# Optimization experiments

Measured on AMD Instinct MI355X. Metric: run time of the kernel, lower is better.

Reference implementation:

```python
import jax, jax.numpy as jnp
import numpy as np

SEQ_LEN = 4_194_304  # number of tokens
INPUT_BITS = 16      # bits per token, MSB first


def setup_inputs() -> dict:
    key = jax.random.key(0)
    # bits in {0,1}; float32 carrier (values exact, matches uint8 bit semantics)
    tokens = jax.random.randint(key, (SEQ_LEN, INPUT_BITS), 0, 2).astype(jnp.float32)
    return {"tokens": tokens}


def reference(tokens):
    # tokens: [seq_len, input_bits], MSB first, entries in {0,1}
    bits = tokens.shape[1]
    # _bits_to_int: val = val*2 + b  ==  dot with [2^(bits-1), ..., 2, 1]
    pow2 = jnp.exp2(jnp.arange(bits - 1, -1, -1, dtype=jnp.float32))  # [bits]
    values = tokens @ pow2  # [seq_len], exact for bits <= 24
    # stable ascending sort == Python list.sort on (value, original_index)
    order = jnp.argsort(values, stable=True)  # [seq_len]
    return tokens[order]  # gather rows by rank
```

## Files before the change

### kernel.cpp

```cpp
#include <hip/hip_runtime.h>
#include <stdint.h>

static constexpr uint32_t SEQN = 4194304u;
static constexpr uint32_t BINS = 65536u;
static constexpr uint32_t QWORDS = BINS / 4u;
static constexpr uint32_t NBLK = 512u;
static constexpr uint32_t NTHR = 1024u;
static constexpr uint32_t ROWS_PER_BLK = SEQN / NBLK;
static constexpr uint32_t NSEG = 8u;

__global__ __launch_bounds__(NTHR) void k_hist_lds(const float4* __restrict__ in4,
                                                   uint32_t* __restrict__ partial) {
  __shared__ uint32_t h[QWORDS];
  uint32_t tid = threadIdx.x, blk = blockIdx.x;
  uint4* hv = (uint4*)h;
  for (uint32_t i = tid; i < QWORDS / 4u; i += NTHR) hv[i] = make_uint4(0u, 0u, 0u, 0u);
  __syncthreads();
  uint32_t row0 = blk * ROWS_PER_BLK;
#pragma unroll 2
  for (uint32_t r = row0 + tid; r < row0 + ROWS_PER_BLK; r += NTHR) {
    const float4* p = in4 + (size_t)r * 4u;
    float4 a = p[0], b = p[1], c = p[2], d = p[3];
    float kf = a.x;
    kf = kf * 2.0f + a.y; kf = kf * 2.0f + a.z; kf = kf * 2.0f + a.w;
    kf = kf * 2.0f + b.x; kf = kf * 2.0f + b.y; kf = kf * 2.0f + b.z; kf = kf * 2.0f + b.w;
    kf = kf * 2.0f + c.x; kf = kf * 2.0f + c.y; kf = kf * 2.0f + c.z; kf = kf * 2.0f + c.w;
    kf = kf * 2.0f + d.x; kf = kf * 2.0f + d.y; kf = kf * 2.0f + d.z; kf = kf * 2.0f + d.w;
    uint32_t key = (uint32_t)kf;
    atomicAdd(&h[key >> 2], 1u << ((key & 3u) << 3));
  }
  __syncthreads();
  uint4* dst = (uint4*)(partial + (size_t)blk * QWORDS);
  for (uint32_t i = tid; i < QWORDS / 4u; i += NTHR) dst[i] = hv[i];
}

__global__ __launch_bounds__(256) void k_reduceA(const uint32_t* __restrict__ partial,
                                                 uint2* __restrict__ seg) {
  uint32_t tid = threadIdx.x, blk = blockIdx.x;
  uint32_t s = blk >> 6, wg = blk & 63u;
  uint32_t w = wg * 256u + tid;
  uint32_t acc_e = 0u, acc_o = 0u;
  uint32_t p0 = s * (NBLK / NSEG);
#pragma unroll 8
  for (uint32_t p = p0; p < p0 + NBLK / NSEG; ++p) {
    uint32_t v = partial[(size_t)p * QWORDS + w];
    acc_e += v & 0x00FF00FFu;
    acc_o += (v >> 8) & 0x00FF00FFu;
  }
  seg[(size_t)s * QWORDS + w] = make_uint2(acc_e, acc_o);
}

__global__ __launch_bounds__(256) void k_scanA(const uint2* __restrict__ seg,
                                               uint32_t* __restrict__ hist,
                                               uint32_t* __restrict__ blkTot) {
  uint32_t tid = threadIdx.x, blk = blockIdx.x;
  uint32_t w = blk * 256u + tid;
  uint32_t e = 0u, o = 0u;
#pragma unroll
  for (uint32_t s = 0; s < NSEG; ++s) {
    uint2 v = seg[(size_t)s * QWORDS + w];
    e += v.x;
    o += v.y;
  }
  uint32_t c0 = e & 0xFFFFu, c2 = e >> 16, c1 = o & 0xFFFFu, c3 = o >> 16;
  ((uint4*)hist)[w] = make_uint4(c0, c1, c2, c3);
  uint32_t ssum = c0 + c1 + c2 + c3;
  for (int d = 1; d < 64; d <<= 1) ssum += __shfl_xor(ssum, d, 64);
  __shared__ uint32_t wt[4];
  if ((tid & 63u) == 0u) wt[tid >> 6] = ssum;
  __syncthreads();
  if (tid == 0u) blkTot[blk] = wt[0] + wt[1] + wt[2] + wt[3];
}

__global__ __launch_bounds__(256) void k_zero(uint32_t* __restrict__ hist) {
  uint32_t i = blockIdx.x * 256u + threadIdx.x;
  if (i < BINS) hist[i] = 0u;
}

__global__ __launch_bounds__(256) void k_hist(const float4* __restrict__ in4,
                                              uint32_t* __restrict__ hist) {
  uint32_t r = blockIdx.x * 256u + threadIdx.x;
  if (r >= SEQN) return;
  uint32_t key = 0u;
#pragma unroll
  for (uint32_t q = 0; q < 4u; ++q) {
    float4 v = in4[(size_t)r * 4u + q];
    uint32_t nib = ((uint32_t)v.x << 3) | ((uint32_t)v.y << 2) |
                   ((uint32_t)v.z << 1) | (uint32_t)v.w;
    key = (key << 4) | nib;
  }
  atomicAdd(&hist[key], 1u);
}

__global__ __launch_bounds__(256) void k_scan1(const uint32_t* __restrict__ hist,
                                               uint32_t* __restrict__ blkTot) {
  uint32_t tid = threadIdx.x, blk = blockIdx.x;
  uint32_t b0 = blk * 1024u + tid * 4u;
  uint32_t s = hist[b0] + hist[b0 + 1] + hist[b0 + 2] + hist[b0 + 3];
  for (int d = 1; d < 64; d <<= 1) s += __shfl_xor(s, d, 64);
  __shared__ uint32_t wt[4];
  if ((tid & 63u) == 0u) wt[tid >> 6] = s;
  __syncthreads();
  if (tid == 0u) blkTot[blk] = wt[0] + wt[1] + wt[2] + wt[3];
}

__global__ __launch_bounds__(64) void k_scan2(uint32_t* __restrict__ blkTot) {
  uint32_t t = threadIdx.x;
  uint32_t v = blkTot[t];
  uint32_t incl = v;
  for (int d = 1; d < 64; d <<= 1) {
    uint32_t n = __shfl_up(incl, d, 64);
    if (t >= (uint32_t)d) incl += n;
  }
  blkTot[t] = incl - v;
}

__global__ __launch_bounds__(256) void k_scan3(const uint32_t* __restrict__ hist,
                                               const uint32_t* __restrict__ blkBase,
                                               uint32_t* __restrict__ offs) {
  uint32_t tid = threadIdx.x, blk = blockIdx.x;
  uint32_t lane = tid & 63u, wid = tid >> 6;
  uint32_t b0 = blk * 1024u + tid * 4u;
  uint4 c = ((const uint4*)hist)[b0 >> 2];
  uint32_t s = c.x + c.y + c.z + c.w;
  uint32_t incl = s;
  for (int d = 1; d < 64; d <<= 1) {
    uint32_t n = __shfl_up(incl, d, 64);
    if (lane >= (uint32_t)d) incl += n;
  }
  __shared__ uint32_t wt[4];
  if (lane == 63u) wt[wid] = incl;
  __syncthreads();
  uint32_t wbase = 0u;
  for (uint32_t w = 0; w < wid; ++w) wbase += wt[w];
  uint32_t base = blkBase[blk] + wbase + (incl - s);
  ((uint4*)offs)[b0 >> 2] = make_uint4(base, base + c.x, base + c.x + c.y,
                                       base + c.x + c.y + c.z);
}

__global__ __launch_bounds__(256) void k_write(const uint32_t* __restrict__ hist,
                                               const uint32_t* __restrict__ offs,
                                               float4* __restrict__ out4) {
  __shared__ uint32_t s_off[32], s_cnt[32];
  uint32_t tid = threadIdx.x, blk = blockIdx.x;
  if (tid < 32u) {
    uint32_t k = blk * 32u + tid;
    s_off[tid] = offs[k];
    s_cnt[tid] = hist[k];
  }
  __syncthreads();
  uint32_t q = tid & 3u;
  for (uint32_t kk = 0; kk < 32u; ++kk) {
    uint32_t k = blk * 32u + kk;
    uint32_t off = s_off[kk], cnt = s_cnt[kk];
    float4 pat;
    pat.x = (float)((k >> (15u - (q * 4u + 0u))) & 1u);
    pat.y = (float)((k >> (15u - (q * 4u + 1u))) & 1u);
    pat.z = (float)((k >> (15u - (q * 4u + 2u))) & 1u);
    pat.w = (float)((k >> (15u - (q * 4u + 3u))) & 1u);
    size_t base = (size_t)off * 4u;
    uint32_t tot = cnt * 4u;
    for (uint32_t j = tid; j < tot; j += 256u) out4[base + j] = pat;
  }
}

extern "C" void kernel_launch(void* const* d_in, const int* in_sizes, int n_in,
                              void* d_out, int out_size, void* d_ws, size_t ws_size,
                              hipStream_t stream) {
  const float4* in4 = (const float4*)d_in[0];
  float4* out4 = (float4*)d_out;
  uint32_t* hist = (uint32_t*)d_ws;
  uint32_t* offs = hist + BINS;
  uint32_t* blkTot = offs + BINS;
  uint32_t* partial = blkTot + 1024u;
  uint2* seg = (uint2*)(partial + (size_t)NBLK * QWORDS);

  size_t need = ((size_t)2 * BINS + 1024u + (size_t)NBLK * QWORDS +
                 (size_t)NSEG * QWORDS * 2u) * 4u;
  if (ws_size >= need) {
    k_hist_lds<<<NBLK, NTHR, 0, stream>>>(in4, partial);
    k_reduceA<<<NSEG * 64, 256, 0, stream>>>(partial, seg);
    k_scanA<<<64, 256, 0, stream>>>(seg, hist, blkTot);
  } else {
    k_zero<<<BINS / 256, 256, 0, stream>>>(hist);
    k_hist<<<SEQN / 256, 256, 0, stream>>>(in4, hist);
    k_scan1<<<64, 256, 0, stream>>>(hist, blkTot);
  }
  k_scan2<<<1, 64, 0, stream>>>(blkTot);
  k_scan3<<<64, 256, 0, stream>>>(hist, blkTot, offs);
  k_write<<<BINS / 32, 256, 0, stream>>>(hist, offs, out4);
}
```

Before: 149.6 us.

## Coalesce histogram loads via quad-lane shuffles and fuse block-total scan into offset scan

The LDS histogram kernel now has each group of four lanes load one row's four float4 pieces contiguously. Each lane builds a nibble, and two xor-shuffles combine the nibbles into the 16-bit key, after which only the leader lane issues the LDS atomic. This makes global loads fully coalesced instead of 64-byte strided per thread. Separately, the single-block block-total scan is folded into the per-block offset scan, where every block redundantly rescans the 64 totals, which removes one kernel launch. In exchange the kernel runs more shuffles and leaves three of every four lanes idle during the atomics.

New measurement: 146.9 us. No clear change (-1.8%).

```diff
diff --git a/kernel.cpp b/kernel.cpp
--- a/kernel.cpp
+++ b/kernel.cpp
@@ -16,18 +16,18 @@
   uint4* hv = (uint4*)h;
   for (uint32_t i = tid; i < QWORDS / 4u; i += NTHR) hv[i] = make_uint4(0u, 0u, 0u, 0u);
   __syncthreads();
-  uint32_t row0 = blk * ROWS_PER_BLK;
-#pragma unroll 2
-  for (uint32_t r = row0 + tid; r < row0 + ROWS_PER_BLK; r += NTHR) {
-    const float4* p = in4 + (size_t)r * 4u;
-    float4 a = p[0], b = p[1], c = p[2], d = p[3];
-    float kf = a.x;
-    kf = kf * 2.0f + a.y; kf = kf * 2.0f + a.z; kf = kf * 2.0f + a.w;
-    kf = kf * 2.0f + b.x; kf = kf * 2.0f + b.y; kf = kf * 2.0f + b.z; kf = kf * 2.0f + b.w;
-    kf = kf * 2.0f + c.x; kf = kf * 2.0f + c.y; kf = kf * 2.0f + c.z; kf = kf * 2.0f + c.w;
-    kf = kf * 2.0f + d.x; kf = kf * 2.0f + d.y; kf = kf * 2.0f + d.z; kf = kf * 2.0f + d.w;
-    uint32_t key = (uint32_t)kf;
-    atomicAdd(&h[key >> 2], 1u << ((key & 3u) << 3));
+  uint32_t q = tid & 3u;
+  uint32_t shift = 12u - (q << 2);
+  bool leader = (q == 0u);
+  const float4* base = in4 + (size_t)blk * (ROWS_PER_BLK * 4u);
+#pragma unroll 4
+  for (uint32_t t = 0; t < (ROWS_PER_BLK * 4u) / NTHR; ++t) {
+    float4 v = base[(size_t)t * NTHR + tid];
+    float nf = ((v.x * 2.0f + v.y) * 2.0f + v.z) * 2.0f + v.w;
+    uint32_t part = ((uint32_t)nf) << shift;
+    part += __shfl_xor(part, 1, 64);
+    part += __shfl_xor(part, 2, 64);
+    if (leader) atomicAdd(&h[part >> 2], 1u << ((part & 3u) << 3));
   }
   __syncthreads();
   uint4* dst = (uint4*)(partial + (size_t)blk * QWORDS);
@@ -83,8 +83,8 @@
   if (r >= SEQN) return;
   uint32_t key = 0u;
 #pragma unroll
-  for (uint32_t q = 0; q < 4u; ++q) {
-    float4 v = in4[(size_t)r * 4u + q];
+  for (uint32_t qq = 0; qq < 4u; ++qq) {
+    float4 v = in4[(size_t)r * 4u + qq];
     uint32_t nib = ((uint32_t)v.x << 3) | ((uint32_t)v.y << 2) |
                    ((uint32_t)v.z << 1) | (uint32_t)v.w;
     key = (key << 4) | nib;
@@ -104,21 +104,22 @@
   if (tid == 0u) blkTot[blk] = wt[0] + wt[1] + wt[2] + wt[3];
 }
 
-__global__ __launch_bounds__(64) void k_scan2(uint32_t* __restrict__ blkTot) {
-  uint32_t t = threadIdx.x;
-  uint32_t v = blkTot[t];
-  uint32_t incl = v;
-  for (int d = 1; d < 64; d <<= 1) {
-    uint32_t n = __shfl_up(incl, d, 64);
-    if (t >= (uint32_t)d) incl += n;
+__global__ __launch_bounds__(256) void k_scanB(const uint32_t* __restrict__ hist,
+                                               const uint32_t* __restrict__ blkTot,
+                                               uint32_t* __restrict__ offs) {
+  __shared__ uint32_t s_base;
+  __shared__ uint32_t wt[4];
+  uint32_t tid = threadIdx.x, blk = blockIdx.x;
+  if (tid < 64u) {
+    uint32_t v = blkTot[tid];
+    uint32_t incl = v;
+    for (int d = 1; d < 64; d <<= 1) {
+      uint32_t n = __shfl_up(incl, d, 64);
+      if (tid >= (uint32_t)d) incl += n;
+    }
+    if (tid == blk) s_base = incl - v;
   }
-  blkTot[t] = incl - v;
-}
-
-__global__ __launch_bounds__(256) void k_scan3(const uint32_t* __restrict__ hist,
-                                               const uint32_t* __restrict__ blkBase,
-                                               uint32_t* __restrict__ offs) {
-  uint32_t tid = threadIdx.x, blk = blockIdx.x;
+  __syncthreads();
   uint32_t lane = tid & 63u, wid = tid >> 6;
   uint32_t b0 = blk * 1024u + tid * 4u;
   uint4 c = ((const uint4*)hist)[b0 >> 2];
@@ -128,12 +129,11 @@
     uint32_t n = __shfl_up(incl, d, 64);
     if (lane >= (uint32_t)d) incl += n;
   }
-  __shared__ uint32_t wt[4];
   if (lane == 63u) wt[wid] = incl;
   __syncthreads();
   uint32_t wbase = 0u;
   for (uint32_t w = 0; w < wid; ++w) wbase += wt[w];
-  uint32_t base = blkBase[blk] + wbase + (incl - s);
+  uint32_t base = s_base + wbase + (incl - s);
   ((uint4*)offs)[b0 >> 2] = make_uint4(base, base + c.x, base + c.x + c.y,
                                        base + c.x + c.y + c.z);
 }
@@ -186,7 +186,6 @@
     k_hist<<<SEQN / 256, 256, 0, stream>>>(in4, hist);
     k_scan1<<<64, 256, 0, stream>>>(hist, blkTot);
   }
-  k_scan2<<<1, 64, 0, stream>>>(blkTot);
-  k_scan3<<<64, 256, 0, stream>>>(hist, blkTot, offs);
+  k_scanB<<<64, 256, 0, stream>>>(hist, blkTot, offs);
   k_write<<<BINS / 32, 256, 0, stream>>>(hist, offs, out4);
 }
```
